# Kernel optimization log

Hardware: AMD Instinct MI355X
Metric: run time of the kernel (lower is better)

Reference implementation:

```python
import jax, jax.numpy as jnp
import numpy as np


def setup_inputs() -> dict:
    key = jax.random.key(0)
    k0, k1, k2, k3, k4 = jax.random.split(key, 5)
    feat0 = jax.random.normal(k0, (32, 256, 56, 56), dtype=jnp.float32)
    feat1 = jax.random.normal(k1, (32, 512, 28, 28), dtype=jnp.float32)
    feat2 = jax.random.normal(k2, (32, 1024, 14, 14), dtype=jnp.float32)
    feat3 = jax.random.normal(k3, (32, 2048, 7, 7), dtype=jnp.float32)
    # Conv2d(3840 -> 1024, kernel_size=1, bias=False): weight [emb, C_total]
    conv_w = jax.random.normal(k4, (1024, 3840), dtype=jnp.float32) * 0.02
    return {"feat0": feat0, "feat1": feat1, "feat2": feat2, "feat3": feat3, "conv_w": conv_w}


def reference(feat0, feat1, feat2, feat3, conv_w):
    # Target spatial size = earliest (largest) level.
    Ht, Wt = feat0.shape[2], feat0.shape[3]

    def up_mean(f):
        # Bilinear upsample (torch Upsample align_corners=False == jax 'bilinear'
        # half-pixel resize), then spatial mean per channel.  Because the 1x1
        # conv and global avg-pool are linear, pooling each upsampled level
        # first and applying the conv on the pooled vector is exactly the
        # same math as conv(concat(upsampled)) followed by avg-pool.
        B, C = f.shape[0], f.shape[1]
        up = jax.image.resize(f, (B, C, Ht, Wt), method='bilinear')  # [B,C,Ht,Wt]
        return jnp.mean(up, axis=(2, 3))  # [B,C]

    v = jnp.concatenate([up_mean(f) for f in (feat0, feat1, feat2, feat3)], axis=1)  # [B, 3840]
    # 1x1 conv (no bias) on pooled vector == GEMM with conv weight, then squeeze.
    return v @ conv_w.T  # [B, emb]
```

## Files before the change

kernel.cpp:

```cpp
#include <hip/hip_runtime.h>


__device__ __forceinline__ float s4(float4 a) { return (a.x + a.y) + (a.z + a.w); }

__device__ __forceinline__ void loadc(float4 (&r)[13], const float4* __restrict__ p, int lane)
{
    #pragma unroll
    for (int i = 0; i < 12; ++i) r[i] = p[lane + (i << 6)];
    r[12] = make_float4(0.f, 0.f, 0.f, 0.f);
    if (lane < 16) r[12] = p[768 + lane];
}

__device__ __forceinline__ float red_f0(const float4 (&r)[13])
{
    float s = 0.f;
    #pragma unroll
    for (int i = 0; i < 13; ++i) s += s4(r[i]);
    #pragma unroll
    for (int o = 32; o; o >>= 1) s += __shfl_xor(s, o);
    return s;
}

__device__ __forceinline__ float4 red_f1(const float4 (&r)[13], int lane)
{
    float a0 = s4(r[0]) + s4(r[1]) + s4(r[2]) + (lane <  4 ? s4(r[3]) : 0.f);
    float a1 = (lane <  4 ? 0.f : s4(r[3])) + s4(r[4]) + s4(r[5])
             + (lane <  8 ? s4(r[6]) : 0.f);
    float a2 = (lane <  8 ? 0.f : s4(r[6])) + s4(r[7]) + s4(r[8])
             + (lane < 12 ? s4(r[9]) : 0.f);
    float a3 = (lane < 12 ? 0.f : s4(r[9])) + s4(r[10]) + s4(r[11]) + s4(r[12]);
    #pragma unroll
    for (int o = 32; o; o >>= 1) {
        a0 += __shfl_xor(a0, o); a1 += __shfl_xor(a1, o);
        a2 += __shfl_xor(a2, o); a3 += __shfl_xor(a3, o);
    }
    return make_float4(a0, a1, a2, a3);
}

__device__ __forceinline__ void store_f1(float* __restrict__ v, int c, float4 a, int lane)
{
    if (lane == 0) {
        int q = (c - 8192) * 4;
        const float inv = 1.f / 784.f;
        *(float4*)&v[(q >> 9) * 3840 + 256 + (q & 511)] =
            make_float4(a.x * inv, a.y * inv, a.z * inv, a.w * inv);
    }
}

__global__ __launch_bounds__(256) void pool_a_kernel(
    const float* __restrict__ f0, const float* __restrict__ f1,
    float* __restrict__ v)
{
    int t = threadIdx.x, w = t >> 6, lane = t & 63;
    int gw = (blockIdx.x << 2) | w;
    int c0 = gw << 2;

    const float4* p = (c0 < 8192)
        ? (const float4*)(f0 + (size_t)c0 * 3136)
        : (const float4*)(f1 + (size_t)(c0 - 8192) * 3136);

    float4 ra[13], rb[13];
    loadc(ra, p, lane);
    loadc(rb, p + 784, lane);

    if (c0 < 8192) {
        float s0 = red_f0(ra); loadc(ra, p + 1568, lane);
        float s1 = red_f0(rb); loadc(rb, p + 2352, lane);
        float s2 = red_f0(ra);
        float s3 = red_f0(rb);
        float val = (lane == 0) ? s0 : (lane == 1) ? s1 : (lane == 2) ? s2 : s3;
        if (lane < 4)
            v[(c0 >> 8) * 3840 + (c0 & 255) + lane] = val * (1.f / 3136.f);
    } else {
        float4 a;
        a = red_f1(ra, lane); loadc(ra, p + 1568, lane);
        store_f1(v, c0 + 0, a, lane);
        a = red_f1(rb, lane); loadc(rb, p + 2352, lane);
        store_f1(v, c0 + 1, a, lane);
        a = red_f1(ra, lane);
        store_f1(v, c0 + 2, a, lane);
        a = red_f1(rb, lane);
        store_f1(v, c0 + 3, a, lane);
    }
}

__global__ __launch_bounds__(256) void pool_bc_kernel(
    const float* __restrict__ f2, const float* __restrict__ f3,
    float* __restrict__ v)
{
    __shared__ float4 ls4[3136];
    float* ls = (float*)ls4;
    int t = threadIdx.x, bid = blockIdx.x;

    const float4* pp = (bid < 512)
        ? (const float4*)(f2 + (size_t)bid * 12544)
        : (const float4*)(f3 + (size_t)(bid - 512) * 12544);
    #pragma unroll
    for (int i = 0; i < 12; ++i) ls4[t + (i << 8)] = pp[t + (i << 8)];
    if (t < 64) ls4[3072 + t] = pp[3072 + t];
    __syncthreads();

    if (bid < 512) {
        int pl = t >> 2, q = t & 3;
        const float* sp = ls + pl * 196 + q * 49;
        float s = 0.f;
        #pragma unroll
        for (int i = 0; i < 48; i += 2) s += sp[i] + sp[i + 1];
        s += sp[48];
        s += __shfl_xor(s, 1); s += __shfl_xor(s, 2);
        if (q == 0) {
            int P = bid * 64 + pl;
            v[(P >> 10) * 3840 + 768 + (P & 1023)] = s * (1.f / 196.f);
        }
    } else {
        const float* sp = ls + t * 49;
        float s = 0.f;
        #pragma unroll
        for (int i = 0; i < 48; i += 2) s += sp[i] + sp[i + 1];
        s += sp[48];
        int P = (bid - 512) * 256 + t;
        v[(P >> 11) * 3840 + 1792 + (P & 2047)] = s * (1.f / 49.f);
    }
}

#define KT 120

__global__ __launch_bounds__(256) void gemm_kernel(
    const float* __restrict__ v, const float* __restrict__ W,
    float* __restrict__ partials)
{
    __shared__ float vs[32][124];
    __shared__ float wsh[64][124];
    int t = threadIdx.x;
    int et = blockIdx.x & 15, ks = blockIdx.x >> 4;
    int e0 = et << 6, k0 = ks * KT;

    {
        float4 tmp[7];
        int row[7], c4[7];
        #pragma unroll
        for (int i = 0; i < 7; ++i) {
            int f = t + (i << 8);
            row[i] = f / 30; c4[i] = f % 30;
            tmp[i] = *(const float4*)&W[(size_t)(e0 + row[i]) * 3840 + k0 + c4[i] * 4];
        }
        float4 tail; int rowt = 0, c4t = 0;
        if (t < 128) {
            int f = t + 1792;
            rowt = f / 30; c4t = f % 30;
            tail = *(const float4*)&W[(size_t)(e0 + rowt) * 3840 + k0 + c4t * 4];
        }
        #pragma unroll
        for (int i = 0; i < 7; ++i)
            *(float4*)&wsh[row[i]][c4[i] * 4] = tmp[i];
        if (t < 128)
            *(float4*)&wsh[rowt][c4t * 4] = tail;
    }
    {
        float4 tmp[3];
        int row[3], c4[3];
        #pragma unroll
        for (int i = 0; i < 3; ++i) {
            int f = t + (i << 8);
            row[i] = f / 30; c4[i] = f % 30;
            tmp[i] = *(const float4*)&v[row[i] * 3840 + k0 + c4[i] * 4];
        }
        float4 tail; int rowt = 0, c4t = 0;
        if (t < 192) {
            int f = t + 768;
            rowt = f / 30; c4t = f % 30;
            tail = *(const float4*)&v[rowt * 3840 + k0 + c4t * 4];
        }
        #pragma unroll
        for (int i = 0; i < 3; ++i)
            *(float4*)&vs[row[i]][c4[i] * 4] = tmp[i];
        if (t < 192)
            *(float4*)&vs[rowt][c4t * 4] = tail;
    }
    __syncthreads();

    int bg = t >> 5, eg = t & 31;
    int b0 = bg << 2;
    float acc[4][2] = {};
    #pragma unroll 5
    for (int k = 0; k < KT; k += 4) {
        float4 vv[4], ww[2];
        #pragma unroll
        for (int i = 0; i < 4; ++i) vv[i] = *(const float4*)&vs[b0 + i][k];
        #pragma unroll
        for (int j = 0; j < 2; ++j) ww[j] = *(const float4*)&wsh[eg + (j << 5)][k];
        #pragma unroll
        for (int i = 0; i < 4; ++i)
            #pragma unroll
            for (int j = 0; j < 2; ++j)
                acc[i][j] += vv[i].x * ww[j].x + vv[i].y * ww[j].y +
                             vv[i].z * ww[j].z + vv[i].w * ww[j].w;
    }

    float* pout = partials + (size_t)ks * 32768 + (size_t)b0 * 1024 + e0 + eg;
    #pragma unroll
    for (int i = 0; i < 4; ++i)
        #pragma unroll
        for (int j = 0; j < 2; ++j)
            pout[i * 1024 + (j << 5)] = acc[i][j];
}

__global__ __launch_bounds__(256) void reduce_kernel(
    const float* __restrict__ partials, float* __restrict__ out)
{
    int idx = blockIdx.x * 256 + threadIdx.x;
    float s0 = 0.f, s1 = 0.f, s2 = 0.f, s3 = 0.f;
    #pragma unroll
    for (int sp = 0; sp < 32; sp += 4) {
        s0 += partials[(sp + 0) * 32768 + idx];
        s1 += partials[(sp + 1) * 32768 + idx];
        s2 += partials[(sp + 2) * 32768 + idx];
        s3 += partials[(sp + 3) * 32768 + idx];
    }
    out[idx] = (s0 + s1) + (s2 + s3);
}

extern "C" void kernel_launch(void* const* d_in, const int* in_sizes, int n_in,
                              void* d_out, int out_size, void* d_ws, size_t ws_size,
                              hipStream_t stream)
{
    const float* f0 = (const float*)d_in[0];
    const float* f1 = (const float*)d_in[1];
    const float* f2 = (const float*)d_in[2];
    const float* f3 = (const float*)d_in[3];
    const float* W  = (const float*)d_in[4];
    float* out = (float*)d_out;

    float* v        = (float*)d_ws;
    float* partials = v + 32 * 3840;

    pool_a_kernel<<<768, 256, 0, stream>>>(f0, f1, v);
    pool_bc_kernel<<<768, 256, 0, stream>>>(f2, f3, v);
    gemm_kernel<<<512, 256, 0, stream>>>(v, W, partials);
    reduce_kernel<<<128, 256, 0, stream>>>(partials, out);
}
```

Baseline: 239.7 us.

## Merge pooling kernels and replace split-K reduce with atomic accumulation

Merges the two pooling kernels into one launch whose extra blocks also zero the output buffer. The GEMM now accumulates its split-K partials straight into the output with atomicAdd, so the partials buffer and separate reduce kernel go away. This cuts two kernel launches and the partials round trip through memory. In exchange, the atomic contention on each output element rises to 32 adds, and the summation order is no longer deterministic. The pooling block also now reserves shared memory even in its register-only branches, which may lower occupancy.

After: 233.4 us. 1.03x faster.

```diff
diff --git a/kernel.cpp b/kernel.cpp
--- a/kernel.cpp
+++ b/kernel.cpp
@@ -47,79 +47,83 @@
     }
 }
 
-__global__ __launch_bounds__(256) void pool_a_kernel(
+__global__ __launch_bounds__(256) void pool_kernel(
     const float* __restrict__ f0, const float* __restrict__ f1,
-    float* __restrict__ v)
-{
-    int t = threadIdx.x, w = t >> 6, lane = t & 63;
-    int gw = (blockIdx.x << 2) | w;
-    int c0 = gw << 2;
-
-    const float4* p = (c0 < 8192)
-        ? (const float4*)(f0 + (size_t)c0 * 3136)
-        : (const float4*)(f1 + (size_t)(c0 - 8192) * 3136);
-
-    float4 ra[13], rb[13];
-    loadc(ra, p, lane);
-    loadc(rb, p + 784, lane);
-
-    if (c0 < 8192) {
-        float s0 = red_f0(ra); loadc(ra, p + 1568, lane);
-        float s1 = red_f0(rb); loadc(rb, p + 2352, lane);
-        float s2 = red_f0(ra);
-        float s3 = red_f0(rb);
-        float val = (lane == 0) ? s0 : (lane == 1) ? s1 : (lane == 2) ? s2 : s3;
-        if (lane < 4)
-            v[(c0 >> 8) * 3840 + (c0 & 255) + lane] = val * (1.f / 3136.f);
+    const float* __restrict__ f2, const float* __restrict__ f3,
+    float* __restrict__ v, float* __restrict__ out)
+{
+    __shared__ float4 ls4[3136];
+    int t = threadIdx.x, bid = blockIdx.x;
+
+    if (bid < 768) {
+        int w = t >> 6, lane = t & 63;
+        int gw = (bid << 2) | w;
+        int c0 = gw << 2;
+
+        const float4* p = (c0 < 8192)
+            ? (const float4*)(f0 + (size_t)c0 * 3136)
+            : (const float4*)(f1 + (size_t)(c0 - 8192) * 3136);
+
+        float4 ra[13], rb[13];
+        loadc(ra, p, lane);
+        loadc(rb, p + 784, lane);
+
+        if (c0 < 8192) {
+            float s0 = red_f0(ra); loadc(ra, p + 1568, lane);
+            float s1 = red_f0(rb); loadc(rb, p + 2352, lane);
+            float s2 = red_f0(ra);
+            float s3 = red_f0(rb);
+            float val = (lane == 0) ? s0 : (lane == 1) ? s1 : (lane == 2) ? s2 : s3;
+            if (lane < 4)
+                v[(c0 >> 8) * 3840 + (c0 & 255) + lane] = val * (1.f / 3136.f);
+        } else {
+            float4 a;
+            a = red_f1(ra, lane); loadc(ra, p + 1568, lane);
+            store_f1(v, c0 + 0, a, lane);
+            a = red_f1(rb, lane); loadc(rb, p + 2352, lane);
+            store_f1(v, c0 + 1, a, lane);
+            a = red_f1(ra, lane);
+            store_f1(v, c0 + 2, a, lane);
+            a = red_f1(rb, lane);
+            store_f1(v, c0 + 3, a, lane);
+        }
+    } else if (bid < 1536) {
+        int b2 = bid - 768;
+        float* ls = (float*)ls4;
+
+        const float4* pp = (b2 < 512)
+            ? (const float4*)(f2 + (size_t)b2 * 12544)
+            : (const float4*)(f3 + (size_t)(b2 - 512) * 12544);
+        #pragma unroll
+        for (int i = 0; i < 12; ++i) ls4[t + (i << 8)] = pp[t + (i << 8)];
+        if (t < 64) ls4[3072 + t] = pp[3072 + t];
+        __syncthreads();
+
+        if (b2 < 512) {
+            int pl = t >> 2, q = t & 3, lane = t & 63;
+            const float* sp = ls + pl * 196 + q * 49;
+            float s = 0.f;
+            #pragma unroll
+            for (int i = 0; i < 48; i += 2) s += sp[i] + sp[i + 1];
+            s += sp[48];
+            s += __shfl_xor(s, 1); s += __shfl_xor(s, 2);
+            (void)lane;
+            if (q == 0) {
+                int P = b2 * 64 + pl;
+                v[(P >> 10) * 3840 + 768 + (P & 1023)] = s * (1.f / 196.f);
+            }
+        } else {
+            const float* sp = ls + t * 49;
+            float s = 0.f;
+            #pragma unroll
+            for (int i = 0; i < 48; i += 2) s += sp[i] + sp[i + 1];
+            s += sp[48];
+            int P = (b2 - 512) * 256 + t;
+            v[(P >> 11) * 3840 + 1792 + (P & 2047)] = s * (1.f / 49.f);
+        }
     } else {
-        float4 a;
-        a = red_f1(ra, lane); loadc(ra, p + 1568, lane);
-        store_f1(v, c0 + 0, a, lane);
-        a = red_f1(rb, lane); loadc(rb, p + 2352, lane);
-        store_f1(v, c0 + 1, a, lane);
-        a = red_f1(ra, lane);
-        store_f1(v, c0 + 2, a, lane);
-        a = red_f1(rb, lane);
-        store_f1(v, c0 + 3, a, lane);
-    }
-}
-
-__global__ __launch_bounds__(256) void pool_bc_kernel(
-    const float* __restrict__ f2, const float* __restrict__ f3,
-    float* __restrict__ v)
-{
-    __shared__ float4 ls4[3136];
-    float* ls = (float*)ls4;
-    int t = threadIdx.x, bid = blockIdx.x;
-
-    const float4* pp = (bid < 512)
-        ? (const float4*)(f2 + (size_t)bid * 12544)
-        : (const float4*)(f3 + (size_t)(bid - 512) * 12544);
-    #pragma unroll
-    for (int i = 0; i < 12; ++i) ls4[t + (i << 8)] = pp[t + (i << 8)];
-    if (t < 64) ls4[3072 + t] = pp[3072 + t];
-    __syncthreads();
-
-    if (bid < 512) {
-        int pl = t >> 2, q = t & 3;
-        const float* sp = ls + pl * 196 + q * 49;
-        float s = 0.f;
-        #pragma unroll
-        for (int i = 0; i < 48; i += 2) s += sp[i] + sp[i + 1];
-        s += sp[48];
-        s += __shfl_xor(s, 1); s += __shfl_xor(s, 2);
-        if (q == 0) {
-            int P = bid * 64 + pl;
-            v[(P >> 10) * 3840 + 768 + (P & 1023)] = s * (1.f / 196.f);
-        }
-    } else {
-        const float* sp = ls + t * 49;
-        float s = 0.f;
-        #pragma unroll
-        for (int i = 0; i < 48; i += 2) s += sp[i] + sp[i + 1];
-        s += sp[48];
-        int P = (bid - 512) * 256 + t;
-        v[(P >> 11) * 3840 + 1792 + (P & 2047)] = s * (1.f / 49.f);
+        int idx = (bid - 1536) * 256 + t;
+        ((float4*)out)[idx] = make_float4(0.f, 0.f, 0.f, 0.f);
     }
 }
 
@@ -127,7 +131,7 @@
 
 __global__ __launch_bounds__(256) void gemm_kernel(
     const float* __restrict__ v, const float* __restrict__ W,
-    float* __restrict__ partials)
+    float* __restrict__ out)
 {
     __shared__ float vs[32][124];
     __shared__ float wsh[64][124];
@@ -197,27 +201,11 @@
                              vv[i].z * ww[j].z + vv[i].w * ww[j].w;
     }
 
-    float* pout = partials + (size_t)ks * 32768 + (size_t)b0 * 1024 + e0 + eg;
     #pragma unroll
     for (int i = 0; i < 4; ++i)
         #pragma unroll
         for (int j = 0; j < 2; ++j)
-            pout[i * 1024 + (j << 5)] = acc[i][j];
-}
-
-__global__ __launch_bounds__(256) void reduce_kernel(
-    const float* __restrict__ partials, float* __restrict__ out)
-{
-    int idx = blockIdx.x * 256 + threadIdx.x;
-    float s0 = 0.f, s1 = 0.f, s2 = 0.f, s3 = 0.f;
-    #pragma unroll
-    for (int sp = 0; sp < 32; sp += 4) {
-        s0 += partials[(sp + 0) * 32768 + idx];
-        s1 += partials[(sp + 1) * 32768 + idx];
-        s2 += partials[(sp + 2) * 32768 + idx];
-        s3 += partials[(sp + 3) * 32768 + idx];
-    }
-    out[idx] = (s0 + s1) + (s2 + s3);
+            atomicAdd(&out[(size_t)(b0 + i) * 1024 + e0 + eg + (j << 5)], acc[i][j]);
 }
 
 extern "C" void kernel_launch(void* const* d_in, const int* in_sizes, int n_in,
@@ -231,11 +219,8 @@
     const float* W  = (const float*)d_in[4];
     float* out = (float*)d_out;
 
-    float* v        = (float*)d_ws;
-    float* partials = v + 32 * 3840;
-
-    pool_a_kernel<<<768, 256, 0, stream>>>(f0, f1, v);
-    pool_bc_kernel<<<768, 256, 0, stream>>>(f2, f3, v);
-    gemm_kernel<<<512, 256, 0, stream>>>(v, W, partials);
-    reduce_kernel<<<128, 256, 0, stream>>>(partials, out);
-}
+    float* v = (float*)d_ws;
+
+    pool_kernel<<<1568, 256, 0, stream>>>(f0, f1, f2, f3, v, out);
+    gemm_kernel<<<512, 256, 0, stream>>>(v, W, out);
+}
```
